# Kernel optimization log

Measured on AMD Instinct MI355X. Metric: run time of the kernel, lower is better.

Reference implementation:

```python
import jax, jax.numpy as jnp
import numpy as np

TOP_K = 2


def setup_inputs() -> dict:
    key = jax.random.key(0)
    k0, k1, k2, k3, k4 = jax.random.split(key, 5)
    B, S, D, F, E = 4, 2048, 2048, 1408, 8
    scale = 0.02
    return {
        "hidden_states": jax.random.normal(k0, (B, S, D), jnp.float32),
        "router_w": jax.random.normal(k1, (D, E), jnp.float32) * scale,
        "w_gate": jax.random.normal(k2, (E, D, F), jnp.float32) * scale,
        "w_up": jax.random.normal(k3, (E, D, F), jnp.float32) * scale,
        "w_down": jax.random.normal(k4, (E, F, D), jnp.float32) * scale,
    }


def reference(hidden_states, router_w, w_gate, w_up, w_down):
    B, S, D = hidden_states.shape
    x = hidden_states.reshape(-1, D)              # [N, D]
    N = x.shape[0]
    E = router_w.shape[-1]

    # ---- Router: softmax over experts, top-k, renormalize top-k probs ----
    logits = x @ router_w                         # [N, E]
    probs = jax.nn.softmax(logits, axis=-1)
    top_w, top_i = jax.lax.top_k(probs, TOP_K)    # [N, K]
    top_w = top_w / jnp.sum(top_w, axis=-1, keepdims=True)

    # Dense gate matrix [N, E]: gate is the (renormalized) routing weight for
    # selected experts, zero otherwise.
    gates = jnp.zeros_like(probs).at[jnp.arange(N)[:, None], top_i].set(top_w)

    # ---- Load-balancing aux loss (Switch-style, averaged over top-k) ----
    f = jnp.mean(jnp.sum(jax.nn.one_hot(top_i, E, dtype=x.dtype), axis=1), axis=0)  # [E] dispatch fraction
    P = jnp.mean(probs, axis=0)                   # [E] mean router prob
    aux_loss = (E / TOP_K) * jnp.sum(f * P)

    # ---- Per-expert SwiGLU FFN, computed as grouped GEMMs over all experts ----
    g = jnp.einsum("nd,edf->enf", x, w_gate)      # [E, N, F]
    u = jnp.einsum("nd,edf->enf", x, w_up)        # [E, N, F]
    h = jax.nn.silu(g) * u                        # [E, N, F]
    expert_out = jnp.einsum("enf,efd->end", h, w_down)  # [E, N, D]

    # ---- Combine: gate-weighted sum over experts ----
    out = jnp.einsum("ne,end->nd", gates, expert_out)   # [N, D]
    return out.reshape(B, S, D), aux_loss
```

## Files before the change

kernel.cpp:

```cpp
#include <hip/hip_runtime.h>

#define N_TOK 8192
#define DIM   2048
#define FFN   1408

#define XB_OFF  0ull
#define HP_OFF  0ull
#define XGP_OFF 49020928ull
#define EO_OFF  49020928ull
#define P1_OFF  120324096ull
#define P2_OFF  212598784ull
#define LPK_OFF 258736128ull
#define TI_OFF  258801664ull
#define TW_OFF  258834432ull
#define TP_OFF  258867200ull
#define ST_OFF  258932736ull

typedef __bf16 bf16x8 __attribute__((ext_vector_type(8)));
typedef float  f32x4  __attribute__((ext_vector_type(4)));
typedef int    int4v  __attribute__((ext_vector_type(4)));
typedef __attribute__((address_space(1))) void as1_void;
typedef __attribute__((address_space(3))) void as3_void;

__device__ __forceinline__ void gload16(const void* g, void* l) {
  __builtin_amdgcn_global_load_lds((as1_void*)g, (as3_void*)l, 16, 0, 0);
}

__device__ __forceinline__ ushort f2bf(float f) {
  unsigned u = __builtin_bit_cast(unsigned, f);
  u += 0x7FFFu + ((u >> 16) & 1u);
  return (ushort)(u >> 16);
}
__device__ __forceinline__ float blo(unsigned w) { return __builtin_bit_cast(float, w << 16); }
__device__ __forceinline__ float bhi(unsigned w) { return __builtin_bit_cast(float, w & 0xffff0000u); }

__device__ __forceinline__ int4v dsread(int addr) {
  int4v d;
  asm volatile("ds_read_b128 %0, %1" : "=v"(d) : "v"(addr));
  return d;
}

#define WAITL() do { asm volatile("s_waitcnt lgkmcnt(0)" ::: "memory"); \
                     __builtin_amdgcn_sched_barrier(0); } while (0)
#define BAR()   __builtin_amdgcn_s_barrier()
#define MFMA16(a, b, c) __builtin_amdgcn_mfma_f32_16x16x32_bf16(a, b, c, 0, 0, 0)
#define BC(x) __builtin_bit_cast(bf16x8, x)

__device__ __forceinline__ int swz(int row, int s) {
  int q = row >> 1;
  int p = (((row & 1) << 2) | s) ^ (q & 7);
  return q * 128 + p * 16;
}

__global__ __launch_bounds__(256) void prep_kernel(
    const float* __restrict__ x, const float* __restrict__ rw,
    ushort* __restrict__ xb, int* __restrict__ topi, float* __restrict__ topw,
    int* __restrict__ cnt, unsigned long long* __restrict__ psum,
    const float* __restrict__ wg, const float* __restrict__ wu,
    const float* __restrict__ wd, char* __restrict__ p1, char* __restrict__ p2)
{
  __shared__ char smem[16640];
  int b = blockIdx.x;

  if (b < 512) {
    int tid = threadIdx.x, lane = tid & 63, wv = tid >> 6;
    float (*sP)[8] = (float(*)[8])smem;
    int   (*sC)[8] = (int(*)[8])(smem + 128);
    float pacc[8]; int cacc[8];
    #pragma unroll
    for (int e = 0; e < 8; ++e) { pacc[e] = 0.f; cacc[e] = 0; }

    #pragma unroll 1
    for (int it = 0; it < 4; ++it) {
      int t = b * 16 + wv * 4 + it;
      const float4* xr = (const float4*)(x + (size_t)t * DIM);
      float acc[8];
      #pragma unroll
      for (int e = 0; e < 8; ++e) acc[e] = 0.f;
      #pragma unroll 1
      for (int i = 0; i < 8; ++i) {
        int j = i * 64 + lane;
        float4 v = xr[j];
        ushort4 o; o.x = f2bf(v.x); o.y = f2bf(v.y); o.z = f2bf(v.z); o.w = f2bf(v.w);
        *(ushort4*)(xb + (size_t)t * DIM + (size_t)j * 4) = o;
        const float* rr = rw + (size_t)j * 32;
        #pragma unroll
        for (int c = 0; c < 4; ++c) {
          float xv = (&v.x)[c];
          const float4* r4 = (const float4*)(rr + c * 8);
          float4 q0 = r4[0], q1 = r4[1];
          acc[0] += xv * q0.x; acc[1] += xv * q0.y; acc[2] += xv * q0.z; acc[3] += xv * q0.w;
          acc[4] += xv * q1.x; acc[5] += xv * q1.y; acc[6] += xv * q1.z; acc[7] += xv * q1.w;
        }
      }
      #pragma unroll
      for (int off = 32; off; off >>= 1) {
        #pragma unroll
        for (int e = 0; e < 8; ++e) acc[e] += __shfl_xor(acc[e], off);
      }
      float m = acc[0];
      #pragma unroll
      for (int e = 1; e < 8; ++e) m = fmaxf(m, acc[e]);
      float p[8], s = 0.f;
      #pragma unroll
      for (int e = 0; e < 8; ++e) { p[e] = __expf(acc[e] - m); s += p[e]; }
      float inv = 1.f / s;
      int i1 = 0; float p1v = p[0];
      #pragma unroll
      for (int e = 1; e < 8; ++e) if (p[e] > p1v) { p1v = p[e]; i1 = e; }
      int i2 = -1; float p2v = -1.f;
      #pragma unroll
      for (int e = 0; e < 8; ++e) if (e != i1 && p[e] > p2v) { p2v = p[e]; i2 = e; }
      float w1 = p1v / (p1v + p2v);
      if (lane == 0) {
        topi[t] = i1 | (i2 << 8);
        topw[t] = w1;
        #pragma unroll
        for (int e = 0; e < 8; ++e) pacc[e] += p[e] * inv;
        cacc[i1]++; cacc[i2]++;
      }
    }
    if (lane == 0) {
      #pragma unroll
      for (int e = 0; e < 8; ++e) { sP[wv][e] = pacc[e]; sC[wv][e] = cacc[e]; }
    }
    __syncthreads();
    if (tid < 8) {
      float ps = sP[0][tid] + sP[1][tid] + sP[2][tid] + sP[3][tid];
      int   cs = sC[0][tid] + sC[1][tid] + sC[2][tid] + sC[3][tid];
      atomicAdd(&cnt[tid], cs);
      atomicAdd(&psum[tid], (unsigned long long)((double)ps * 1099511627776.0));
    }
  } else if (b < 11776) {
    int q_ = b - 512;
    int j = q_ & 63, rest = q_ >> 6;
    int tn = rest % 22, e = rest / 22;
    float (*tg)[65] = (float(*)[65])smem;
    float (*tu)[65] = (float(*)[65])(smem + 8320);
    int t = threadIdx.x;
    const float* gs = wg + ((size_t)e * DIM + j * 32) * FFN + tn * 64;
    const float* us = wu + ((size_t)e * DIM + j * 32) * FFN + tn * 64;
    #pragma unroll
    for (int k2 = 0; k2 < 2; ++k2) {
      int idx = t + k2 * 256;
      int kk = idx >> 4, fq = idx & 15;
      *(float4*)&tg[kk][fq * 4] = *(const float4*)(gs + (size_t)kk * FFN + fq * 4);
      *(float4*)&tu[kk][fq * 4] = *(const float4*)(us + (size_t)kk * FFN + fq * 4);
    }
    __syncthreads();
    char* dst = p1 + ((size_t)((e * 22 + tn) * 64 + j)) * 8192;
    #pragma unroll
    for (int k2 = 0; k2 < 2; ++k2) {
      int L = t + k2 * 256;
      int q = L >> 3, v = (L & 7) ^ (q & 7);
      int r = 2 * q + (v >> 2), s = v & 3;
      const float* col = (r < 64) ? &tg[s * 8][r] : &tu[s * 8][r - 64];
      ushort u8[8];
      #pragma unroll
      for (int i = 0; i < 8; ++i) u8[i] = f2bf(col[i * 65]);
      *(ushort4*)(dst + (size_t)L * 16) = *(ushort4*)&u8[0];
      *(ushort4*)(dst + (size_t)L * 16 + 8) = *(ushort4*)&u8[4];
    }
  } else {
    int q_ = b - 11776;
    int j = q_ % 44, rest = q_ / 44;
    int tn = rest & 15, e = rest >> 4;
    float (*t2)[129] = (float(*)[129])smem;
    int t = threadIdx.x;
    const float* src = wd + ((size_t)e * FFN + j * 32) * DIM + tn * 128;
    #pragma unroll
    for (int k2 = 0; k2 < 4; ++k2) {
      int idx = t + k2 * 256;
      int kk = idx >> 5, dq = idx & 31;
      *(float4*)&t2[kk][dq * 4] = *(const float4*)(src + (size_t)kk * DIM + dq * 4);
    }
    __syncthreads();
    char* dst = p2 + ((size_t)((e * 16 + tn) * 44 + j)) * 8192;
    #pragma unroll
    for (int k2 = 0; k2 < 2; ++k2) {
      int L = t + k2 * 256;
      int q = L >> 3, v = (L & 7) ^ (q & 7);
      int r = 2 * q + (v >> 2), s = v & 3;
      ushort u8[8];
      #pragma unroll
      for (int i = 0; i < 8; ++i) u8[i] = f2bf(t2[s * 8 + i][r]);
      *(ushort4*)(dst + (size_t)L * 16) = *(ushort4*)&u8[0];
      *(ushort4*)(dst + (size_t)L * 16 + 8) = *(ushort4*)&u8[4];
    }
  }
}

__global__ void scan_aux_kernel(int* __restrict__ stats,
                                const unsigned long long* __restrict__ psum,
                                float* __restrict__ aux_out)
{
  if (threadIdx.x == 0 && blockIdx.x == 0) {
    int b = 0, tb = 0;
    for (int e = 0; e < 8; ++e) {
      stats[8 + e] = b; stats[16 + e] = b; stats[24 + e] = tb;
      tb += (stats[e] + 127) >> 7;
      b += stats[e];
    }
    stats[32] = tb;
    double s = 0.0;
    for (int e = 0; e < 8; ++e)
      s += (double)stats[e] * ((double)psum[e] * (1.0 / 1099511627776.0));
    aux_out[0] = (float)(4.0 * s / ((double)N_TOK * (double)N_TOK));
  }
}

__global__ __launch_bounds__(256) void place_kernel(
    const int* __restrict__ topi, int* __restrict__ stats,
    int* __restrict__ lpk, int2* __restrict__ tpos)
{
  int t = blockIdx.x * 256 + threadIdx.x;
  if (t >= N_TOK) return;
  int pk = topi[t];
  int e1 = pk & 0xff, e2 = (pk >> 8) & 0xff;
  int p1 = atomicAdd(&stats[8 + e1], 1);
  lpk[p1] = t;
  int p2 = atomicAdd(&stats[8 + e2], 1);
  lpk[p2] = t;
  tpos[t] = make_int2(p1, p2);
}

__global__ __launch_bounds__(256) void gather_x_kernel(
    const ushort* __restrict__ xb, const int* __restrict__ lpk,
    const int* __restrict__ stats, char* __restrict__ xgp)
{
  int b = blockIdx.x;
  int tile = b >> 1;
  if (tile >= stats[32]) return;
  int e = 0;
  #pragma unroll
  for (int k = 1; k < 8; ++k) if (tile >= stats[24 + k]) e = k;
  int tloc = tile - stats[24 + e];
  int abase = stats[16 + e], Me = stats[e];
  int half = b & 1;
  int lane = threadIdx.x & 63, wv = threadIdx.x >> 6;
  char* base = xgp + (size_t)tile * 64 * 8192;
  #pragma unroll 1
  for (int r = half * 64 + wv; r < half * 64 + 64; r += 4) {
    int lrow = tloc * 128 + r;
    bool valid = lrow < Me;
    const char* src = (const char*)xb + (valid ? (size_t)lpk[abase + lrow] * (DIM * 2) : 0);
    int q = r >> 1;
    #pragma unroll
    for (int it = 0; it < 4; ++it) {
      int c16 = it * 64 + lane;
      int j = c16 >> 2, s = c16 & 3;
      uint4 v;
      if (valid) v = *(const uint4*)(src + c16 * 16);
      else       v = make_uint4(0, 0, 0, 0);
      int p = (((r & 1) << 2) | s) ^ (q & 7);
      *(uint4*)(base + (size_t)j * 8192 + q * 128 + p * 16) = v;
    }
  }
}


#define GSTAGE(AC, BC_, BUF) do { int d_ = (BUF) * 16384 + wv * 2048; \
  gload16((AC) + wv * 2048 + lane * 16, sm + d_); \
  gload16((AC) + wv * 2048 + 1024 + lane * 16, sm + d_ + 1024); \
  gload16((BC_) + wv * 2048 + lane * 16, sm + d_ + 8192); \
  gload16((BC_) + wv * 2048 + 1024 + lane * 16, sm + d_ + 8192 + 1024); \
} while (0)

#define KLOOP(NCH) \
  GSTAGE(aP, bP, 0); \
  _Pragma("unroll 1") \
  for (int j = 0; j < (NCH); ++j) { \
    if (j + 1 < (NCH)) { \
      GSTAGE(aP + (size_t)(j + 1) * 8192, bP + (size_t)(j + 1) * 8192, (j + 1) & 1); \
      asm volatile("s_waitcnt vmcnt(4)" ::: "memory"); \
    } else { \
      asm volatile("s_waitcnt vmcnt(0)" ::: "memory"); \
    } \
    BAR(); \
    int sb = (j & 1) * 16384; \
    int4v va[4], vb[4]; \
    _Pragma("unroll") for (int n = 0; n < 4; ++n) vb[n] = dsread(sb + adB[n]); \
    _Pragma("unroll") for (int m = 0; m < 4; ++m) va[m] = dsread(sb + adA[m]); \
    WAITL(); \
    __builtin_amdgcn_s_setprio(1); \
    _Pragma("unroll") for (int m = 0; m < 4; ++m) \
      _Pragma("unroll") for (int n = 0; n < 4; ++n) \
        acc[m][n] = MFMA16(BC(va[m]), BC(vb[n]), acc[m][n]); \
    __builtin_amdgcn_s_setprio(0); \
    BAR(); \
  }

__global__ __launch_bounds__(256, 4) void gemm_gu_kernel(
    const char* __restrict__ xgp, const char* __restrict__ p1,
    const int* __restrict__ stats, char* __restrict__ hp)
{
  int bid = blockIdx.x;
  int e = bid & 7;
  int Ll = bid >> 3;
  int tm = Ll / 22, tn = Ll % 22;
  int Me = stats[e];
  if (tm * 128 >= Me) return;
  int tb = stats[24 + e];

  __shared__ char sm[32768];
  int tid = threadIdx.x, lane = tid & 63, wv = tid >> 6;
  const char* aP = xgp + (size_t)(tb + tm) * 64 * 8192;
  const char* bP = p1 + (size_t)((e * 22 + tn) * 64) * 8192;

  int wm = wv >> 1, wn = wv & 1, s = lane >> 4;
  int adA[4], adB[4];
  #pragma unroll
  for (int m = 0; m < 4; ++m) adA[m] = swz(wm * 64 + m * 16 + (lane & 15), s);
  #pragma unroll
  for (int n = 0; n < 4; ++n) adB[n] = 8192 + swz(wn * 64 + n * 16 + (lane & 15), s);

  f32x4 acc[4][4];
  #pragma unroll
  for (int m = 0; m < 4; ++m)
    #pragma unroll
    for (int n = 0; n < 4; ++n) acc[m][n] = (f32x4){0, 0, 0, 0};

  KLOOP(64);

  float* u_lds = (float*)sm;
  if (wn == 1) {
    #pragma unroll
    for (int m = 0; m < 4; ++m)
      #pragma unroll
      for (int n = 0; n < 4; ++n)
        #pragma unroll
        for (int r = 0; r < 4; ++r) {
          int row = wm * 64 + m * 16 + (lane >> 4) * 4 + r;
          int c = n * 16 + (lane & 15);
          u_lds[row * 64 + c] = acc[m][n][r];
        }
  }
  __syncthreads();
  if (wn == 0) {
    char* hb = hp + (size_t)(tb + tm) * 44 * 8192;
    #pragma unroll
    for (int m = 0; m < 4; ++m)
      #pragma unroll
      for (int n = 0; n < 4; ++n)
        #pragma unroll
        for (int r = 0; r < 4; ++r) {
          int row = wm * 64 + m * 16 + (lane >> 4) * 4 + r;
          int c = n * 16 + (lane & 15);
          float g = acc[m][n][r];
          float u = u_lds[row * 64 + c];
          float hv = g * u / (1.f + __expf(-g));
          int f = tn * 64 + c;
          int j2 = f >> 5, s2 = (f >> 3) & 3, i2 = f & 7;
          int q = row >> 1;
          int p = (((row & 1) << 2) | s2) ^ (q & 7);
          *(ushort*)(hb + (size_t)j2 * 8192 + q * 128 + p * 16 + i2 * 2) = f2bf(hv);
        }
  }
}

__global__ __launch_bounds__(256, 4) void gemm_down_kernel(
    const char* __restrict__ hp, const char* __restrict__ p2,
    const int* __restrict__ stats, ushort* __restrict__ eo)
{
  int bid = blockIdx.x;
  int e = bid & 7;
  int Ll = bid >> 3;
  int tm = Ll >> 4, tn = Ll & 15;
  int Me = stats[e];
  if (tm * 128 >= Me) return;
  int tb = stats[24 + e], abase = stats[16 + e];

  __shared__ char sm[32768];
  int tid = threadIdx.x, lane = tid & 63, wv = tid >> 6;
  const char* aP = hp + (size_t)(tb + tm) * 44 * 8192;
  const char* bP = p2 + (size_t)((e * 16 + tn) * 44) * 8192;

  int wm = wv >> 1, wn = wv & 1, s = lane >> 4;
  int adA[4], adB[4];
  #pragma unroll
  for (int m = 0; m < 4; ++m) adA[m] = swz(wm * 64 + m * 16 + (lane & 15), s);
  #pragma unroll
  for (int n = 0; n < 4; ++n) adB[n] = 8192 + swz(wn * 64 + n * 16 + (lane & 15), s);

  f32x4 acc[4][4];
  #pragma unroll
  for (int m = 0; m < 4; ++m)
    #pragma unroll
    for (int n = 0; n < 4; ++n) acc[m][n] = (f32x4){0, 0, 0, 0};

  KLOOP(44);

  int c0 = lane & 15, r0 = (lane >> 4) * 4;
  #pragma unroll
  for (int m = 0; m < 4; ++m) {
    #pragma unroll
    for (int r = 0; r < 4; ++r) {
      int lrow = tm * 128 + wm * 64 + m * 16 + r0 + r;
      if (lrow < Me) {
        ushort* dst = eo + (size_t)(abase + lrow) * DIM + tn * 128 + wn * 64 + c0;
        #pragma unroll
        for (int n = 0; n < 4; ++n) dst[n * 16] = f2bf(acc[m][n][r]);
      }
    }
  }
}

__global__ __launch_bounds__(256) void combine_kernel(
    const ushort* __restrict__ eo, const int2* __restrict__ tpos,
    const float* __restrict__ topw, float* __restrict__ out)
{
  int t = blockIdx.x;
  int2 tp = tpos[t];
  float w1 = topw[t], w2 = 1.f - w1;
  const uint4* r1 = (const uint4*)(eo + (size_t)tp.x * DIM);
  const uint4* r2 = (const uint4*)(eo + (size_t)tp.y * DIM);
  float4* o = (float4*)(out + (size_t)t * DIM);
  int i = threadIdx.x;
  uint4 a = r1[i], b = r2[i];
  float4 c0, c1;
  c0.x = w1 * blo(a.x) + w2 * blo(b.x);  c0.y = w1 * bhi(a.x) + w2 * bhi(b.x);
  c0.z = w1 * blo(a.y) + w2 * blo(b.y);  c0.w = w1 * bhi(a.y) + w2 * bhi(b.y);
  c1.x = w1 * blo(a.z) + w2 * blo(b.z);  c1.y = w1 * bhi(a.z) + w2 * bhi(b.z);
  c1.z = w1 * blo(a.w) + w2 * blo(b.w);  c1.w = w1 * bhi(a.w) + w2 * bhi(b.w);
  o[i * 2] = c0;
  o[i * 2 + 1] = c1;
}

extern "C" void kernel_launch(void* const* d_in, const int* in_sizes, int n_in,
                              void* d_out, int out_size, void* d_ws, size_t ws_size,
                              hipStream_t stream)
{
  const float* x  = (const float*)d_in[0];
  const float* rw = (const float*)d_in[1];
  const float* wg = (const float*)d_in[2];
  const float* wu = (const float*)d_in[3];
  const float* wd = (const float*)d_in[4];
  float* out = (float*)d_out;

  char* ws = (char*)d_ws;
  ushort* xb   = (ushort*)(ws + XB_OFF);
  char*   hp   = ws + HP_OFF;
  char*   xgp  = ws + XGP_OFF;
  ushort* eo   = (ushort*)(ws + EO_OFF);
  char*   p1   = ws + P1_OFF;
  char*   p2   = ws + P2_OFF;
  int*    lpk  = (int*)(ws + LPK_OFF);
  int*    topi = (int*)(ws + TI_OFF);
  float*  topw = (float*)(ws + TW_OFF);
  int2*   tpos = (int2*)(ws + TP_OFF);
  int*    stats = (int*)(ws + ST_OFF);
  unsigned long long* psum = (unsigned long long*)(ws + ST_OFF + 192);

  hipMemsetAsync(ws + ST_OFF, 0, 256, stream);

  prep_kernel<<<17408, 256, 0, stream>>>(x, rw, xb, topi, topw, stats, psum,
                                         wg, wu, wd, p1, p2);
  scan_aux_kernel<<<1, 64, 0, stream>>>(stats, psum, out + (size_t)out_size - 1);
  place_kernel<<<32, 256, 0, stream>>>(topi, stats, lpk, tpos);

  gather_x_kernel<<<272, 256, 0, stream>>>(xb, lpk, stats, xgp);

  gemm_gu_kernel<<<5632, 256, 0, stream>>>(xgp, p1, stats, hp);
  gemm_down_kernel<<<4096, 256, 0, stream>>>(hp, p2, stats, eo);

  combine_kernel<<<8192, 256, 0, stream>>>(eo, tpos, topw, out);
}
```

Measured before the change: 534.5 us.

## Enlarge GEMM tiles to 256x128 with per-wave full-width N

Both expert GEMMs now compute 256-row by 128-column tiles: each of the four waves owns 64 rows across all 128 columns (4x8 MFMA accumulators). This raises arithmetic intensity per LDS load and halves the number of blocks. In the gate/up kernel a wave now holds both the gate and up halves, so the SwiGLU epilogue reads them from registers instead of staging through LDS and a block barrier. The cost is more accumulator registers, 48KB of LDS, occupancy lowered to 2 blocks per CU, and more wasted rows when an expert's token count is not a multiple of 256.

```diff
diff --git a/kernel.cpp b/kernel.cpp
--- a/kernel.cpp
+++ b/kernel.cpp
@@ -259,38 +259,42 @@
 }
 
 
-#define GSTAGE(AC, BC_, BUF) do { int d_ = (BUF) * 16384 + wv * 2048; \
-  gload16((AC) + wv * 2048 + lane * 16, sm + d_); \
-  gload16((AC) + wv * 2048 + 1024 + lane * 16, sm + d_ + 1024); \
-  gload16((BC_) + wv * 2048 + lane * 16, sm + d_ + 8192); \
-  gload16((BC_) + wv * 2048 + 1024 + lane * 16, sm + d_ + 8192 + 1024); \
+#define GSTAGE(J, BUF) do { \
+  size_t go_ = (size_t)(J) * 8192 + wv * 2048 + lane * 16; \
+  int d_ = (BUF) * 24576 + wv * 2048; \
+  gload16(aP0 + go_,        sm + d_); \
+  gload16(aP0 + go_ + 1024, sm + d_ + 1024); \
+  gload16(aP1 + go_,        sm + d_ + 8192); \
+  gload16(aP1 + go_ + 1024, sm + d_ + 8192 + 1024); \
+  gload16(bP + go_,         sm + d_ + 16384); \
+  gload16(bP + go_ + 1024,  sm + d_ + 16384 + 1024); \
 } while (0)
 
 #define KLOOP(NCH) \
-  GSTAGE(aP, bP, 0); \
+  GSTAGE(0, 0); \
   _Pragma("unroll 1") \
   for (int j = 0; j < (NCH); ++j) { \
     if (j + 1 < (NCH)) { \
-      GSTAGE(aP + (size_t)(j + 1) * 8192, bP + (size_t)(j + 1) * 8192, (j + 1) & 1); \
-      asm volatile("s_waitcnt vmcnt(4)" ::: "memory"); \
+      GSTAGE(j + 1, (j + 1) & 1); \
+      asm volatile("s_waitcnt vmcnt(6)" ::: "memory"); \
     } else { \
       asm volatile("s_waitcnt vmcnt(0)" ::: "memory"); \
     } \
     BAR(); \
-    int sb = (j & 1) * 16384; \
-    int4v va[4], vb[4]; \
-    _Pragma("unroll") for (int n = 0; n < 4; ++n) vb[n] = dsread(sb + adB[n]); \
+    int sb = (j & 1) * 24576; \
+    int4v va[4], vb[8]; \
+    _Pragma("unroll") for (int n = 0; n < 8; ++n) vb[n] = dsread(sb + adB[n]); \
     _Pragma("unroll") for (int m = 0; m < 4; ++m) va[m] = dsread(sb + adA[m]); \
     WAITL(); \
     __builtin_amdgcn_s_setprio(1); \
     _Pragma("unroll") for (int m = 0; m < 4; ++m) \
-      _Pragma("unroll") for (int n = 0; n < 4; ++n) \
+      _Pragma("unroll") for (int n = 0; n < 8; ++n) \
         acc[m][n] = MFMA16(BC(va[m]), BC(vb[n]), acc[m][n]); \
     __builtin_amdgcn_s_setprio(0); \
     BAR(); \
   }
 
-__global__ __launch_bounds__(256, 4) void gemm_gu_kernel(
+__global__ __launch_bounds__(256, 2) void gemm_gu_kernel(
     const char* __restrict__ xgp, const char* __restrict__ p1,
     const int* __restrict__ stats, char* __restrict__ hp)
 {
@@ -299,66 +303,59 @@
   int Ll = bid >> 3;
   int tm = Ll / 22, tn = Ll % 22;
   int Me = stats[e];
-  if (tm * 128 >= Me) return;
+  if (tm * 256 >= Me) return;
   int tb = stats[24 + e];
 
-  __shared__ char sm[32768];
+  __shared__ char sm[49152];
   int tid = threadIdx.x, lane = tid & 63, wv = tid >> 6;
-  const char* aP = xgp + (size_t)(tb + tm) * 64 * 8192;
+  const char* aP0 = xgp + (size_t)(tb + tm * 2) * 64 * 8192;
+  const char* aP1 = aP0 + 64 * 8192;
   const char* bP = p1 + (size_t)((e * 22 + tn) * 64) * 8192;
 
-  int wm = wv >> 1, wn = wv & 1, s = lane >> 4;
-  int adA[4], adB[4];
-  #pragma unroll
-  for (int m = 0; m < 4; ++m) adA[m] = swz(wm * 64 + m * 16 + (lane & 15), s);
-  #pragma unroll
-  for (int n = 0; n < 4; ++n) adB[n] = 8192 + swz(wn * 64 + n * 16 + (lane & 15), s);
-
-  f32x4 acc[4][4];
+  int s = lane >> 4;
+  int adA[4], adB[8];
+  #pragma unroll
+  for (int m = 0; m < 4; ++m) {
+    int row = wv * 64 + m * 16 + (lane & 15);
+    adA[m] = (row >> 7) * 8192 + swz(row & 127, s);
+  }
+  #pragma unroll
+  for (int n = 0; n < 8; ++n) adB[n] = 16384 + swz(n * 16 + (lane & 15), s);
+
+  f32x4 acc[4][8];
   #pragma unroll
   for (int m = 0; m < 4; ++m)
     #pragma unroll
-    for (int n = 0; n < 4; ++n) acc[m][n] = (f32x4){0, 0, 0, 0};
+    for (int n = 0; n < 8; ++n) acc[m][n] = (f32x4){0, 0, 0, 0};
 
   KLOOP(64);
 
-  float* u_lds = (float*)sm;
-  if (wn == 1) {
-    #pragma unroll
-    for (int m = 0; m < 4; ++m)
-      #pragma unroll
-      for (int n = 0; n < 4; ++n)
+  int r0 = (lane >> 4) * 4, cl = lane & 15;
+  #pragma unroll
+  for (int m = 0; m < 4; ++m) {
+    #pragma unroll
+    for (int r = 0; r < 4; ++r) {
+      int row = wv * 64 + m * 16 + r0 + r;
+      if (tm * 256 + row < Me) {
+        char* hb = hp + (size_t)(tb + tm * 2 + (row >> 7)) * 44 * 8192;
+        int lr = row & 127;
+        int q = lr >> 1;
         #pragma unroll
-        for (int r = 0; r < 4; ++r) {
-          int row = wm * 64 + m * 16 + (lane >> 4) * 4 + r;
-          int c = n * 16 + (lane & 15);
-          u_lds[row * 64 + c] = acc[m][n][r];
-        }
-  }
-  __syncthreads();
-  if (wn == 0) {
-    char* hb = hp + (size_t)(tb + tm) * 44 * 8192;
-    #pragma unroll
-    for (int m = 0; m < 4; ++m)
-      #pragma unroll
-      for (int n = 0; n < 4; ++n)
-        #pragma unroll
-        for (int r = 0; r < 4; ++r) {
-          int row = wm * 64 + m * 16 + (lane >> 4) * 4 + r;
-          int c = n * 16 + (lane & 15);
+        for (int n = 0; n < 4; ++n) {
           float g = acc[m][n][r];
-          float u = u_lds[row * 64 + c];
+          float u = acc[m][n + 4][r];
           float hv = g * u / (1.f + __expf(-g));
-          int f = tn * 64 + c;
+          int f = tn * 64 + n * 16 + cl;
           int j2 = f >> 5, s2 = (f >> 3) & 3, i2 = f & 7;
-          int q = row >> 1;
-          int p = (((row & 1) << 2) | s2) ^ (q & 7);
+          int p = (((lr & 1) << 2) | s2) ^ (q & 7);
           *(ushort*)(hb + (size_t)j2 * 8192 + q * 128 + p * 16 + i2 * 2) = f2bf(hv);
         }
-  }
-}
-
-__global__ __launch_bounds__(256, 4) void gemm_down_kernel(
+      }
+    }
+  }
+}
+
+__global__ __launch_bounds__(256, 2) void gemm_down_kernel(
     const char* __restrict__ hp, const char* __restrict__ p2,
     const int* __restrict__ stats, ushort* __restrict__ eo)
 {
@@ -367,26 +364,30 @@
   int Ll = bid >> 3;
   int tm = Ll >> 4, tn = Ll & 15;
   int Me = stats[e];
-  if (tm * 128 >= Me) return;
+  if (tm * 256 >= Me) return;
   int tb = stats[24 + e], abase = stats[16 + e];
 
-  __shared__ char sm[32768];
+  __shared__ char sm[49152];
   int tid = threadIdx.x, lane = tid & 63, wv = tid >> 6;
-  const char* aP = hp + (size_t)(tb + tm) * 44 * 8192;
+  const char* aP0 = hp + (size_t)(tb + tm * 2) * 44 * 8192;
+  const char* aP1 = aP0 + 44 * 8192;
   const char* bP = p2 + (size_t)((e * 16 + tn) * 44) * 8192;
 
-  int wm = wv >> 1, wn = wv & 1, s = lane >> 4;
-  int adA[4], adB[4];
-  #pragma unroll
-  for (int m = 0; m < 4; ++m) adA[m] = swz(wm * 64 + m * 16 + (lane & 15), s);
-  #pragma unroll
-  for (int n = 0; n < 4; ++n) adB[n] = 8192 + swz(wn * 64 + n * 16 + (lane & 15), s);
-
-  f32x4 acc[4][4];
+  int s = lane >> 4;
+  int adA[4], adB[8];
+  #pragma unroll
+  for (int m = 0; m < 4; ++m) {
+    int row = wv * 64 + m * 16 + (lane & 15);
+    adA[m] = (row >> 7) * 8192 + swz(row & 127, s);
+  }
+  #pragma unroll
+  for (int n = 0; n < 8; ++n) adB[n] = 16384 + swz(n * 16 + (lane & 15), s);
+
+  f32x4 acc[4][8];
   #pragma unroll
   for (int m = 0; m < 4; ++m)
     #pragma unroll
-    for (int n = 0; n < 4; ++n) acc[m][n] = (f32x4){0, 0, 0, 0};
+    for (int n = 0; n < 8; ++n) acc[m][n] = (f32x4){0, 0, 0, 0};
 
   KLOOP(44);
 
@@ -395,11 +396,11 @@
   for (int m = 0; m < 4; ++m) {
     #pragma unroll
     for (int r = 0; r < 4; ++r) {
-      int lrow = tm * 128 + wm * 64 + m * 16 + r0 + r;
+      int lrow = tm * 256 + wv * 64 + m * 16 + r0 + r;
       if (lrow < Me) {
-        ushort* dst = eo + (size_t)(abase + lrow) * DIM + tn * 128 + wn * 64 + c0;
+        ushort* dst = eo + (size_t)(abase + lrow) * DIM + tn * 128 + c0;
         #pragma unroll
-        for (int n = 0; n < 4; ++n) dst[n * 16] = f2bf(acc[m][n][r]);
+        for (int n = 0; n < 8; ++n) dst[n * 16] = f2bf(acc[m][n][r]);
       }
     }
   }
@@ -460,8 +461,8 @@
 
   gather_x_kernel<<<272, 256, 0, stream>>>(xb, lpk, stats, xgp);
 
-  gemm_gu_kernel<<<5632, 256, 0, stream>>>(xgp, p1, stats, hp);
-  gemm_down_kernel<<<4096, 256, 0, stream>>>(hp, p2, stats, eo);
+  gemm_gu_kernel<<<2816, 256, 0, stream>>>(xgp, p1, stats, hp);
+  gemm_down_kernel<<<2048, 256, 0, stream>>>(hp, p2, stats, eo);
 
   combine_kernel<<<8192, 256, 0, stream>>>(eo, tpos, topw, out);
 }
```

Result: no change. 533.5 us (-0.2%).
